# Performance work log

Measured on AMD Instinct MI355X. Metric: run time of the kernel, lower is better.

The kernel has to match this reference:

```python
import jax, jax.numpy as jnp
import numpy as np

V, TB, L, H, D, HD, FF = 50257, 1024, 6, 12, 768, 64, 4 * 768
B, T = 2, 1024
EOS = 50256


def _layernorm(x, g, b, eps=1e-5):
    mu = x.mean(-1, keepdims=True)
    var = ((x - mu) ** 2).mean(-1, keepdims=True)
    return (x - mu) * jax.lax.rsqrt(var + eps) * g + b


def setup_inputs() -> dict:
    key = jax.random.key(0)
    ks = jax.random.split(key, 10)
    resid_std = 0.02 * (2 * L) ** (-0.5)

    def n(k, shape, std=0.02):
        return (std * jax.random.normal(k, shape)).astype(jnp.float32)

    return {
        "idx": jax.random.randint(ks[0], (B, T), 0, V, dtype=jnp.int32),
        "targets": jax.random.randint(ks[1], (B, T), 0, V, dtype=jnp.int32),
        "token_emb": n(ks[2], (V, D)),           # tied with head
        "pos_emb": n(ks[3], (1, TB, D)),
        "ln1_g": jnp.ones((L, D), jnp.float32),
        "ln1_b": jnp.zeros((L, D), jnp.float32),
        "ln2_g": jnp.ones((L, D), jnp.float32),
        "ln2_b": jnp.zeros((L, D), jnp.float32),
        "W_qkv": n(ks[4], (L, D, 3 * D)),
        "b_qkv": jnp.zeros((L, 3 * D), jnp.float32),
        "W_proj": n(ks[5], (L, D, D), resid_std),
        "b_proj": jnp.zeros((L, D), jnp.float32),
        "W_fc1": n(ks[6], (L, D, FF)),
        "b_fc1": jnp.zeros((L, FF), jnp.float32),
        "W_fc2": n(ks[7], (L, FF, D), resid_std),
        "b_fc2": jnp.zeros((L, D), jnp.float32),
        "lnf_g": jnp.ones((D,), jnp.float32),
        "lnf_b": jnp.zeros((D,), jnp.float32),
    }


def reference(idx, targets, token_emb, pos_emb, ln1_g, ln1_b, ln2_g, ln2_b,
              W_qkv, b_qkv, W_proj, b_proj, W_fc1, b_fc1, W_fc2, b_fc2,
              lnf_g, lnf_b):
    Bc, Tc = idx.shape
    x = token_emb[idx] + pos_emb[:, :Tc, :]  # [B,T,D]; dropout=0 -> identity

    # document-boundary causal mask: same_doc & causal
    is_eos = (idx == EOS).astype(jnp.int32)
    doc_id = jnp.cumsum(is_eos, axis=1) - is_eos          # [B,T]
    same_doc = doc_id[:, :, None] == doc_id[:, None, :]   # [B,T,T]
    causal = jnp.tril(jnp.ones((Tc, Tc), dtype=bool))
    mask = same_doc & causal                               # [B,T,T]
    scale = 1.0 / float(np.sqrt(HD))

    def block(x, p):
        g1, b1, Wq, bq, Wp, bp, g2, b2, Wf1, bf1, Wf2, bf2 = p
        h = _layernorm(x, g1, b1)
        qkv = (h @ Wq + bq).reshape(Bc, Tc, 3, H, HD)
        q = qkv[:, :, 0].transpose(0, 2, 1, 3)  # [B,H,T,hd]
        k = qkv[:, :, 1].transpose(0, 2, 1, 3)
        v = qkv[:, :, 2].transpose(0, 2, 1, 3)
        att = jnp.einsum('bhqd,bhkd->bhqk', q, k) * scale
        att = jnp.where(mask[:, None, :, :], att, -jnp.inf)
        att = jax.nn.softmax(att, axis=-1)
        y = jnp.einsum('bhqk,bhkd->bhqd', att, v)
        y = y.transpose(0, 2, 1, 3).reshape(Bc, Tc, D)
        x = x + (y @ Wp + bp)
        h2 = _layernorm(x, g2, b2)
        x = x + (jax.nn.gelu(h2 @ Wf1 + bf1, approximate=False) @ Wf2 + bf2)
        return x, None

    x, _ = jax.lax.scan(block, x, (ln1_g, ln1_b, W_qkv, b_qkv, W_proj, b_proj,
                                   ln2_g, ln2_b, W_fc1, b_fc1, W_fc2, b_fc2))
    x = _layernorm(x, lnf_g, lnf_b)
    logits = x @ token_emb.T  # tied head, no bias
    logp = jax.nn.log_softmax(logits, axis=-1)
    tgt = targets.astype(jnp.int32)[..., None]
    loss = -jnp.take_along_axis(logp, tgt, axis=-1).mean()
    return logits, loss
```

## Files before the change

kernel.cpp:

```cpp
#include <hip/hip_runtime.h>
#include <hip/hip_bf16.h>
#include <math.h>

#define V_ 50257
#define L_ 6
#define H_ 12
#define D_ 768
#define HD_ 64
#define FF_ 3072
#define B_ 2
#define T_ 1024
#define NTOK (B_*T_)
#define EOS_ 50256
#define QBLK 64
#define KVB 64
#define NS2 393
#define QS3 (3*D_)

typedef __attribute__((ext_vector_type(8))) short s16x8;
typedef __attribute__((ext_vector_type(4))) float f32x4;

__device__ __forceinline__ short f2bf(float f) {
  __hip_bfloat16 h = __float2bfloat16(f);
  return *reinterpret_cast<short*>(&h);
}

__device__ __forceinline__ void gl_lds16(const void* g, void* l) {
  __builtin_amdgcn_global_load_lds(
      (const __attribute__((address_space(1))) unsigned int*)g,
      (__attribute__((address_space(3))) unsigned int*)l, 16, 0, 0);
}

__global__ void k_embed(const int* __restrict__ idx, const float* __restrict__ tok,
                        const float* __restrict__ pos, float* __restrict__ x) {
  int gid = blockIdx.x * blockDim.x + threadIdx.x;
  const int total = NTOK * D_;
  if (gid >= total) return;
  int row = gid / D_;
  int d = gid - row * D_;
  int t = row & (T_ - 1);
  x[gid] = tok[(size_t)idx[row] * D_ + d] + pos[t * D_ + d];
}

__global__ void k_docid(const int* __restrict__ idx, int* __restrict__ doc) {
  int b = threadIdx.x;
  if (b >= B_) return;
  int c = 0;
  for (int t = 0; t < T_; ++t) {
    int e = (idx[b*T_ + t] == EOS_) ? 1 : 0;
    doc[b*T_ + t] = c;
    c += e;
  }
}

__global__ void k_cast_tok(const float* __restrict__ in,
                           __hip_bfloat16* __restrict__ out, long n8) {
  long i = (long)blockIdx.x*blockDim.x + threadIdx.x;
  long stride = (long)gridDim.x*blockDim.x;
  for (; i < n8; i += stride) {
    const float4* src = (const float4*)(in + i*8);
    float4 v0 = src[0], v1 = src[1];
    s16x8 s;
    s[0]=f2bf(v0.x); s[1]=f2bf(v0.y); s[2]=f2bf(v0.z); s[3]=f2bf(v0.w);
    s[4]=f2bf(v1.x); s[5]=f2bf(v1.y); s[6]=f2bf(v1.z); s[7]=f2bf(v1.w);
    *(s16x8*)((short*)out + i*8) = s;
  }
}

__global__ void k_ln(const float* __restrict__ x, const float* __restrict__ g,
                     const float* __restrict__ b, __hip_bfloat16* __restrict__ out) {
  int row = blockIdx.x;
  const float* xr = x + (size_t)row * D_;
  int lane = threadIdx.x;
  float vals[D_/64];
  float s = 0.f;
  #pragma unroll
  for (int i = 0; i < D_/64; ++i) { vals[i] = xr[lane + i*64]; s += vals[i]; }
  #pragma unroll
  for (int o = 1; o < 64; o <<= 1) s += __shfl_xor(s, o);
  float mu = s * (1.f/D_);
  float v = 0.f;
  #pragma unroll
  for (int i = 0; i < D_/64; ++i) { float d0 = vals[i]-mu; v += d0*d0; }
  #pragma unroll
  for (int o = 1; o < 64; o <<= 1) v += __shfl_xor(v, o);
  float inv = rsqrtf(v * (1.f/D_) + 1e-5f);
  #pragma unroll
  for (int i = 0; i < D_/64; ++i) {
    int d = lane + i*64;
    out[(size_t)row*D_ + d] = __float2bfloat16((vals[i]-mu)*inv*g[d] + b[d]);
  }
}

__global__ void k_wt(const float* __restrict__ in, __hip_bfloat16* __restrict__ out,
                     int K, int N) {
  __shared__ float tile[32][33];
  int l = blockIdx.z;
  const float* src = in + (size_t)l*K*N;
  __hip_bfloat16* dst = out + (size_t)l*N*K;
  int n0 = blockIdx.x*32, k0 = blockIdx.y*32;
  int tx = threadIdx.x, ty = threadIdx.y;
  #pragma unroll
  for (int i = 0; i < 4; ++i)
    tile[ty + i*8][tx] = src[(size_t)(k0 + ty + i*8)*N + n0 + tx];
  __syncthreads();
  #pragma unroll
  for (int i = 0; i < 4; ++i)
    dst[(size_t)(n0 + ty + i*8)*K + k0 + tx] = __float2bfloat16(tile[tx][ty + i*8]);
}

__global__ __launch_bounds__(256) void k_mfma_nt(
    const __hip_bfloat16* __restrict__ A,
    const __hip_bfloat16* __restrict__ Bh,
    const float* __restrict__ Bf,
    const float* __restrict__ bias,
    const float* resid,
    float* outf, __hip_bfloat16* outh,
    int M, int N, int K, int gelu)
{
  __shared__ __align__(16) short lds_a[128*64];
  __shared__ __align__(16) short lds_b[128*64];
  const int t = threadIdx.x;
  const int m0 = blockIdx.y * 128;
  const int n0 = blockIdx.x * 128;
  const int lane = t & 63;
  const int wid = t >> 6;
  const int wm = (wid >> 1) * 64;
  const int wn = (wid & 1) * 64;
  const int lrow = lane & 15;
  const int lkb = (lane >> 4) * 16;
  const int wbase = (t & 192) * 16;

  f32x4 acc[4][4];
  #pragma unroll
  for (int i = 0; i < 4; ++i)
    #pragma unroll
    for (int j = 0; j < 4; ++j)
      acc[i][j] = (f32x4){0.f, 0.f, 0.f, 0.f};

  for (int k0 = 0; k0 < K; k0 += 64) {
    #pragma unroll
    for (int p = 0; p < 4; ++p) {
      int c = p*256 + t;
      int row = c >> 3;
      int colb = (c & 7) << 4;
      const char* src = (const char*)A + ((size_t)(m0+row)*K + k0)*2 + (colb ^ ((row & 7) << 4));
      gl_lds16(src, (char*)lds_a + p*4096 + wbase);
    }
    if (Bh) {
      #pragma unroll
      for (int p = 0; p < 4; ++p) {
        int c = p*256 + t;
        int row = c >> 3;
        int colb = (c & 7) << 4;
        const char* src = (const char*)Bh + ((size_t)(n0+row)*K + k0)*2 + (colb ^ ((row & 7) << 4));
        gl_lds16(src, (char*)lds_b + p*4096 + wbase);
      }
    } else {
      #pragma unroll
      for (int p = 0; p < 4; ++p) {
        int c = p*256 + t;
        int row = c >> 3;
        int colb = (c & 7) << 4;
        int gn = n0 + row;
        s16x8 s = {0,0,0,0,0,0,0,0};
        if (gn < N) {
          const char* src = (const char*)Bf + ((size_t)gn*K + k0)*4 + colb*2;
          float4 v0 = *(const float4*)src;
          float4 v1 = *(const float4*)(src + 16);
          s[0]=f2bf(v0.x); s[1]=f2bf(v0.y); s[2]=f2bf(v0.z); s[3]=f2bf(v0.w);
          s[4]=f2bf(v1.x); s[5]=f2bf(v1.y); s[6]=f2bf(v1.z); s[7]=f2bf(v1.w);
        }
        int dst = (row*128 + colb) ^ ((row & 7) << 4);
        *(s16x8*)((char*)lds_b + dst) = s;
      }
    }
    __syncthreads();
    #pragma unroll
    for (int ks = 0; ks < 2; ++ks) {
      s16x8 af[4], bfr[4];
      #pragma unroll
      for (int f = 0; f < 4; ++f) {
        int row = wm + f*16 + lrow;
        int off = (row*128 + ks*64 + lkb) ^ ((row & 7) << 4);
        af[f] = *(const s16x8*)((const char*)lds_a + off);
      }
      #pragma unroll
      for (int f = 0; f < 4; ++f) {
        int row = wn + f*16 + lrow;
        int off = (row*128 + ks*64 + lkb) ^ ((row & 7) << 4);
        bfr[f] = *(const s16x8*)((const char*)lds_b + off);
      }
      #pragma unroll
      for (int fm = 0; fm < 4; ++fm)
        #pragma unroll
        for (int fn = 0; fn < 4; ++fn)
          acc[fm][fn] = __builtin_amdgcn_mfma_f32_16x16x32_bf16(
              af[fm], bfr[fn], acc[fm][fn], 0, 0, 0);
    }
    __syncthreads();
  }
  const int crow = (lane >> 4) * 4;
  #pragma unroll
  for (int fm = 0; fm < 4; ++fm) {
    #pragma unroll
    for (int fn = 0; fn < 4; ++fn) {
      int col = n0 + wn + fn*16 + lrow;
      if (col >= N) continue;
      #pragma unroll
      for (int r = 0; r < 4; ++r) {
        int row = m0 + wm + fm*16 + crow + r;
        float v = acc[fm][fn][r];
        if (bias) v += bias[col];
        if (gelu) v = 0.5f * v * (1.f + erff(v * 0.70710678118654752f));
        if (resid) v += resid[(size_t)row*N + col];
        if (outf) outf[(size_t)row*N + col] = v;
        else      outh[(size_t)row*N + col] = __float2bfloat16(v);
      }
    }
  }
}

__global__ __launch_bounds__(256) void k_mfma_nt64(
    const __hip_bfloat16* __restrict__ A,
    const __hip_bfloat16* __restrict__ Bh,
    const float* __restrict__ bias,
    const float* resid,
    float* outf,
    int M, int N, int K)
{
  __shared__ __align__(16) short lds_a[64*64];
  __shared__ __align__(16) short lds_b[64*64];
  const int t = threadIdx.x;
  const int m0 = blockIdx.y * 64;
  const int n0 = blockIdx.x * 64;
  const int lane = t & 63;
  const int wid = t >> 6;
  const int wm = (wid >> 1) * 32;
  const int wn = (wid & 1) * 32;
  const int lrow = lane & 15;
  const int lkb = (lane >> 4) * 16;
  const int wbase = (t & 192) * 16;

  f32x4 acc[2][2];
  #pragma unroll
  for (int i = 0; i < 2; ++i)
    #pragma unroll
    for (int j = 0; j < 2; ++j)
      acc[i][j] = (f32x4){0.f, 0.f, 0.f, 0.f};

  for (int k0 = 0; k0 < K; k0 += 64) {
    #pragma unroll
    for (int p = 0; p < 2; ++p) {
      int c = p*256 + t;
      int row = c >> 3;
      int colb = (c & 7) << 4;
      const char* srcA = (const char*)A + ((size_t)(m0+row)*K + k0)*2 + (colb ^ ((row & 7) << 4));
      gl_lds16(srcA, (char*)lds_a + p*4096 + wbase);
    }
    #pragma unroll
    for (int p = 0; p < 2; ++p) {
      int c = p*256 + t;
      int row = c >> 3;
      int colb = (c & 7) << 4;
      const char* srcB = (const char*)Bh + ((size_t)(n0+row)*K + k0)*2 + (colb ^ ((row & 7) << 4));
      gl_lds16(srcB, (char*)lds_b + p*4096 + wbase);
    }
    __syncthreads();
    #pragma unroll
    for (int ks = 0; ks < 2; ++ks) {
      s16x8 af[2], bfr[2];
      #pragma unroll
      for (int f = 0; f < 2; ++f) {
        int row = wm + f*16 + lrow;
        int off = (row*128 + ks*64 + lkb) ^ ((row & 7) << 4);
        af[f] = *(const s16x8*)((const char*)lds_a + off);
      }
      #pragma unroll
      for (int f = 0; f < 2; ++f) {
        int row = wn + f*16 + lrow;
        int off = (row*128 + ks*64 + lkb) ^ ((row & 7) << 4);
        bfr[f] = *(const s16x8*)((const char*)lds_b + off);
      }
      #pragma unroll
      for (int fm = 0; fm < 2; ++fm)
        #pragma unroll
        for (int fn = 0; fn < 2; ++fn)
          acc[fm][fn] = __builtin_amdgcn_mfma_f32_16x16x32_bf16(
              af[fm], bfr[fn], acc[fm][fn], 0, 0, 0);
    }
    __syncthreads();
  }
  const int crow = (lane >> 4) * 4;
  #pragma unroll
  for (int fm = 0; fm < 2; ++fm) {
    #pragma unroll
    for (int fn = 0; fn < 2; ++fn) {
      int col = n0 + wn + fn*16 + lrow;
      #pragma unroll
      for (int r = 0; r < 4; ++r) {
        int row = m0 + wm + fm*16 + crow + r;
        float v = acc[fm][fn][r] + bias[col];
        if (resid) v += resid[(size_t)row*N + col];
        outf[(size_t)row*N + col] = v;
      }
    }
  }
}

__global__ __launch_bounds__(256) void k_logits(
    const __hip_bfloat16* __restrict__ A,
    const __hip_bfloat16* __restrict__ Bh,
    const float* __restrict__ Bf,
    float* __restrict__ C,
    float2* __restrict__ part)
{
  __shared__ __align__(16) short lds_a[128*64];
  __shared__ __align__(16) short lds_b[128*64];
  const int t = threadIdx.x;
  const int bid = blockIdx.x;
  const int lid = (bid & 7) * (NS2*16/8) + (bid >> 3);
  const int m0 = (lid & 15) * 128;
  const int nt = lid >> 4;
  const int n0 = nt * 128;
  const int lane = t & 63;
  const int wid = t >> 6;
  const int wm = (wid >> 1) * 64;
  const int wn = (wid & 1) * 64;
  const int lrow = lane & 15;
  const int lkb = (lane >> 4) * 16;
  const int wbase = (t & 192) * 16;

  f32x4 acc[4][4];
  #pragma unroll
  for (int i = 0; i < 4; ++i)
    #pragma unroll
    for (int j = 0; j < 4; ++j)
      acc[i][j] = (f32x4){0.f, 0.f, 0.f, 0.f};

  for (int k0 = 0; k0 < 768; k0 += 64) {
    #pragma unroll
    for (int p = 0; p < 4; ++p) {
      int c = p*256 + t;
      int row = c >> 3;
      int colb = (c & 7) << 4;
      const char* src = (const char*)A + ((size_t)(m0+row)*768 + k0)*2 + (colb ^ ((row & 7) << 4));
      gl_lds16(src, (char*)lds_a + p*4096 + wbase);
    }
    if (Bh) {
      #pragma unroll
      for (int p = 0; p < 4; ++p) {
        int c = p*256 + t;
        int row = c >> 3;
        int colb = (c & 7) << 4;
        const char* src = (const char*)Bh + ((size_t)(n0+row)*768 + k0)*2 + (colb ^ ((row & 7) << 4));
        gl_lds16(src, (char*)lds_b + p*4096 + wbase);
      }
    } else {
      #pragma unroll
      for (int p = 0; p < 4; ++p) {
        int c = p*256 + t;
        int row = c >> 3;
        int colb = (c & 7) << 4;
        int gn = n0 + row;
        s16x8 s = {0,0,0,0,0,0,0,0};
        if (gn < V_) {
          const char* src = (const char*)Bf + ((size_t)gn*768 + k0)*4 + colb*2;
          float4 v0 = *(const float4*)src;
          float4 v1 = *(const float4*)(src + 16);
          s[0]=f2bf(v0.x); s[1]=f2bf(v0.y); s[2]=f2bf(v0.z); s[3]=f2bf(v0.w);
          s[4]=f2bf(v1.x); s[5]=f2bf(v1.y); s[6]=f2bf(v1.z); s[7]=f2bf(v1.w);
        }
        int dst = (row*128 + colb) ^ ((row & 7) << 4);
        *(s16x8*)((char*)lds_b + dst) = s;
      }
    }
    __syncthreads();
    #pragma unroll
    for (int ks = 0; ks < 2; ++ks) {
      s16x8 af[4], bfr[4];
      #pragma unroll
      for (int f = 0; f < 4; ++f) {
        int row = wm + f*16 + lrow;
        int off = (row*128 + ks*64 + lkb) ^ ((row & 7) << 4);
        af[f] = *(const s16x8*)((const char*)lds_a + off);
      }
      #pragma unroll
      for (int f = 0; f < 4; ++f) {
        int row = wn + f*16 + lrow;
        int off = (row*128 + ks*64 + lkb) ^ ((row & 7) << 4);
        bfr[f] = *(const s16x8*)((const char*)lds_b + off);
      }
      #pragma unroll
      for (int fm = 0; fm < 4; ++fm)
        #pragma unroll
        for (int fn = 0; fn < 4; ++fn)
          acc[fm][fn] = __builtin_amdgcn_mfma_f32_16x16x32_bf16(
              af[fm], bfr[fn], acc[fm][fn], 0, 0, 0);
    }
    __syncthreads();
  }
  const int crow = (lane >> 4) * 4;
  bool valid[4];
  #pragma unroll
  for (int fn = 0; fn < 4; ++fn) valid[fn] = (n0 + wn + fn*16 + lrow) < V_;
  float2* red = (float2*)lds_a;
  #pragma unroll
  for (int fm = 0; fm < 4; ++fm) {
    #pragma unroll
    for (int r = 0; r < 4; ++r) {
      int rit = wm + fm*16 + crow + r;
      int row = m0 + rit;
      float m = -1e30f;
      #pragma unroll
      for (int fn = 0; fn < 4; ++fn) {
        if (valid[fn]) {
          float v = acc[fm][fn][r];
          __builtin_nontemporal_store(v, &C[(size_t)row*V_ + n0 + wn + fn*16 + lrow]);
          m = fmaxf(m, v);
        }
      }
      #pragma unroll
      for (int o = 1; o < 16; o <<= 1) m = fmaxf(m, __shfl_xor(m, o));
      float s = 0.f;
      #pragma unroll
      for (int fn = 0; fn < 4; ++fn)
        if (valid[fn]) s += __expf(acc[fm][fn][r] - m);
      #pragma unroll
      for (int o = 1; o < 16; o <<= 1) s += __shfl_xor(s, o);
      if (lrow == 0) red[rit*2 + (wid & 1)] = make_float2(m, s);
    }
  }
  __syncthreads();
  if (t < 128) {
    float2 a = red[t*2], b = red[t*2 + 1];
    float mn = fmaxf(a.x, b.x);
    float S = a.y*__expf(a.x - mn) + b.y*__expf(b.x - mn);
    part[(size_t)(m0 + t)*NS2 + nt] = make_float2(mn, S);
  }
}

__global__ void k_rowloss2(const float2* __restrict__ part,
                           const float* __restrict__ logits,
                           const int* __restrict__ tgt, float* __restrict__ rl) {
  int row = blockIdx.x;
  int lane = threadIdx.x;
  float M = -1e30f, S = 0.f;
  for (int i = lane; i < NS2; i += 64) {
    float2 p = part[(size_t)row*NS2 + i];
    float mn = fmaxf(M, p.x);
    S = S*__expf(M - mn) + p.y*__expf(p.x - mn);
    M = mn;
  }
  #pragma unroll
  for (int o = 1; o < 64; o <<= 1) {
    float Mo = __shfl_xor(M, o);
    float So = __shfl_xor(S, o);
    float mn = fmaxf(M, Mo);
    S = S*__expf(M - mn) + So*__expf(Mo - mn);
    M = mn;
  }
  if (lane == 0)
    rl[row] = (logf(S) + M) - logits[(size_t)row*V_ + tgt[row]];
}

__global__ __launch_bounds__(256) void k_fattn(
    const __hip_bfloat16* __restrict__ qkv, const int* __restrict__ doc,
    __hip_bfloat16* __restrict__ y)
{
  __shared__ __align__(16) short q_lds[QBLK*64];
  __shared__ __align__(16) short k_lds[KVB*64];
  __shared__ __align__(16) short vt_lds[64*KVB];
  __shared__ __align__(16) short p_lds[4][16*64];
  __shared__ int doc_k[KVB];
  const int t = threadIdx.x;
  const int lane = t & 63;
  const int w = t >> 6;
  const int q0 = blockIdx.x * QBLK;
  const int h = blockIdx.y, b = blockIdx.z;
  const int lrow = lane & 15;
  const int lgrp = lane >> 4;
  const int crow = lgrp * 4;
  const int wbase = (t & 192) * 16;
  const short* qp = (const short*)qkv;

  #pragma unroll
  for (int p = 0; p < 2; ++p) {
    int c = p*256 + t;
    int row = c >> 3;
    int colb = (c & 7) << 4;
    const char* src = (const char*)(qp + ((size_t)(b*T_ + q0 + row))*QS3 + h*HD_)
                      + (colb ^ ((row & 7) << 4));
    gl_lds16(src, (char*)q_lds + p*4096 + wbase);
  }
  int docq[4];
  #pragma unroll
  for (int r = 0; r < 4; ++r)
    docq[r] = doc[b*T_ + q0 + w*16 + crow + r];
  __syncthreads();

  float m_r[4], l_r[4];
  #pragma unroll
  for (int r = 0; r < 4; ++r) { m_r[r] = -1e30f; l_r[r] = 0.f; }
  f32x4 o[4];
  #pragma unroll
  for (int fd = 0; fd < 4; ++fd) o[fd] = (f32x4){0.f,0.f,0.f,0.f};

  const int ntiles = q0/KVB + 1;
  for (int kt = 0; kt < ntiles; ++kt) {
    const int kv0 = kt * KVB;
    #pragma unroll
    for (int p = 0; p < 2; ++p) {
      int c = p*256 + t;
      int row = c >> 3;
      int colb = (c & 7) << 4;
      const char* src = (const char*)(qp + ((size_t)(b*T_ + kv0 + row))*QS3 + D_ + h*HD_)
                        + (colb ^ ((row & 7) << 4));
      gl_lds16(src, (char*)k_lds + p*4096 + wbase);
    }
    #pragma unroll
    for (int p = 0; p < 2; ++p) {
      int c = p*256 + t;
      int kvr = c >> 3, d0 = (c & 7)*8;
      s16x8 s = *(const s16x8*)(qp + ((size_t)(b*T_ + kv0 + kvr))*QS3 + 2*D_ + h*HD_ + d0);
      #pragma unroll
      for (int j = 0; j < 8; ++j) {
        int d = d0 + j;
        int off = (d*128 + kvr*2) ^ ((d & 7) << 4);
        *(short*)((char*)vt_lds + off) = s[j];
      }
    }
    if (t < KVB) doc_k[t] = doc[b*T_ + kv0 + t];
    __syncthreads();

    f32x4 sfr[4];
    #pragma unroll
    for (int fn = 0; fn < 4; ++fn) sfr[fn] = (f32x4){0.f,0.f,0.f,0.f};
    #pragma unroll
    for (int ks = 0; ks < 2; ++ks) {
      int arow = w*16 + lrow;
      s16x8 af = *(const s16x8*)((const char*)q_lds +
                 ((arow*128 + lgrp*16 + ks*64) ^ ((arow & 7) << 4)));
      #pragma unroll
      for (int fn = 0; fn < 4; ++fn) {
        int brow = fn*16 + lrow;
        s16x8 bf = *(const s16x8*)((const char*)k_lds +
                   ((brow*128 + lgrp*16 + ks*64) ^ ((brow & 7) << 4)));
        sfr[fn] = __builtin_amdgcn_mfma_f32_16x16x32_bf16(af, bf, sfr[fn], 0, 0, 0);
      }
    }
    int dk[4];
    #pragma unroll
    for (int fn = 0; fn < 4; ++fn) dk[fn] = doc_k[fn*16 + lrow];
    float rowmax[4] = {-1e30f, -1e30f, -1e30f, -1e30f};
    #pragma unroll
    for (int fn = 0; fn < 4; ++fn) {
      int col = kv0 + fn*16 + lrow;
      #pragma unroll
      for (int r = 0; r < 4; ++r) {
        int qrow = q0 + w*16 + crow + r;
        bool ok = (col <= qrow) && (dk[fn] == docq[r]);
        float v = ok ? sfr[fn][r] * 0.125f : -1e30f;
        sfr[fn][r] = v;
        rowmax[r] = fmaxf(rowmax[r], v);
      }
    }
    #pragma unroll
    for (int r = 0; r < 4; ++r) {
      float v = rowmax[r];
      #pragma unroll
      for (int off = 1; off < 16; off <<= 1) v = fmaxf(v, __shfl_xor(v, off));
      rowmax[r] = v;
    }
    float alpha[4], psum[4];
    #pragma unroll
    for (int r = 0; r < 4; ++r) {
      float mn = fmaxf(m_r[r], rowmax[r]);
      alpha[r] = __expf(m_r[r] - mn);
      m_r[r] = mn;
      psum[r] = 0.f;
    }
    #pragma unroll
    for (int fn = 0; fn < 4; ++fn) {
      #pragma unroll
      for (int r = 0; r < 4; ++r) {
        float sv = sfr[fn][r];
        float p = (sv < -5e29f) ? 0.f : __expf(sv - m_r[r]);
        psum[r] += p;
        int rl_ = crow + r;
        int off = (rl_*128 + (fn*16 + lrow)*2) ^ ((rl_ & 7) << 4);
        *(short*)((char*)p_lds[w] + off) = f2bf(p);
      }
    }
    #pragma unroll
    for (int r = 0; r < 4; ++r) {
      float v = psum[r];
      #pragma unroll
      for (int off = 1; off < 16; off <<= 1) v += __shfl_xor(v, off);
      l_r[r] = l_r[r]*alpha[r] + v;
    }
    #pragma unroll
    for (int fd = 0; fd < 4; ++fd)
      #pragma unroll
      for (int r = 0; r < 4; ++r)
        o[fd][r] *= alpha[r];
    __syncthreads();
    #pragma unroll
    for (int ks = 0; ks < 2; ++ks) {
      s16x8 af = *(const s16x8*)((const char*)p_lds[w] +
                 ((lrow*128 + lgrp*16 + ks*64) ^ ((lrow & 7) << 4)));
      #pragma unroll
      for (int fd = 0; fd < 4; ++fd) {
        int brow = fd*16 + lrow;
        s16x8 bf = *(const s16x8*)((const char*)vt_lds +
                   ((brow*128 + lgrp*16 + ks*64) ^ ((brow & 7) << 4)));
        o[fd] = __builtin_amdgcn_mfma_f32_16x16x32_bf16(af, bf, o[fd], 0, 0, 0);
      }
    }
    __syncthreads();
  }
  #pragma unroll
  for (int r = 0; r < 4; ++r) {
    float inv = 1.f / l_r[r];
    int rowg = b*T_ + q0 + w*16 + crow + r;
    #pragma unroll
    for (int fd = 0; fd < 4; ++fd) {
      int col = h*HD_ + fd*16 + lrow;
      y[(size_t)rowg*D_ + col] = __float2bfloat16(o[fd][r] * inv);
    }
  }
}

__global__ void k_rowloss(const float* __restrict__ logits,
                          const int* __restrict__ tgt, float* __restrict__ rl) {
  __shared__ float red[4];
  int row = blockIdx.x;
  const float* lr = logits + (size_t)row * V_;
  int tid = threadIdx.x;
  float m = -1e30f;
  for (int v = tid; v < V_; v += 256) m = fmaxf(m, lr[v]);
  #pragma unroll
  for (int o = 1; o < 64; o <<= 1) m = fmaxf(m, __shfl_xor(m, o));
  if ((tid & 63) == 0) red[tid >> 6] = m;
  __syncthreads();
  m = fmaxf(fmaxf(red[0], red[1]), fmaxf(red[2], red[3]));
  __syncthreads();
  float s = 0.f;
  for (int v = tid; v < V_; v += 256) s += __expf(lr[v] - m);
  #pragma unroll
  for (int o = 1; o < 64; o <<= 1) s += __shfl_xor(s, o);
  if ((tid & 63) == 0) red[tid >> 6] = s;
  __syncthreads();
  if (tid == 0) {
    s = red[0]+red[1]+red[2]+red[3];
    rl[row] = (logf(s) + m) - lr[tgt[row]];
  }
}

__global__ void k_loss(const float* __restrict__ rl, float* __restrict__ out) {
  __shared__ float red[4];
  int tid = threadIdx.x;
  float s = 0.f;
  for (int i = tid; i < NTOK; i += 256) s += rl[i];
  #pragma unroll
  for (int o = 1; o < 64; o <<= 1) s += __shfl_xor(s, o);
  if ((tid & 63) == 0) red[tid >> 6] = s;
  __syncthreads();
  if (tid == 0) {
    s = red[0]+red[1]+red[2]+red[3];
    out[0] = s / (float)NTOK;
  }
}

extern "C" void kernel_launch(void* const* d_in, const int* in_sizes, int n_in,
                              void* d_out, int out_size, void* d_ws, size_t ws_size,
                              hipStream_t stream) {
  const int*   idx   = (const int*)d_in[0];
  const int*   tgt   = (const int*)d_in[1];
  const float* tok   = (const float*)d_in[2];
  const float* pos   = (const float*)d_in[3];
  const float* ln1_g = (const float*)d_in[4];
  const float* ln1_b = (const float*)d_in[5];
  const float* ln2_g = (const float*)d_in[6];
  const float* ln2_b = (const float*)d_in[7];
  const float* W_qkv = (const float*)d_in[8];
  const float* b_qkv = (const float*)d_in[9];
  const float* W_proj= (const float*)d_in[10];
  const float* b_proj= (const float*)d_in[11];
  const float* W_fc1 = (const float*)d_in[12];
  const float* b_fc1 = (const float*)d_in[13];
  const float* W_fc2 = (const float*)d_in[14];
  const float* b_fc2 = (const float*)d_in[15];
  const float* lnf_g = (const float*)d_in[16];
  const float* lnf_b = (const float*)d_in[17];

  float* out = (float*)d_out;

  char* ob = (char*)d_out;
  float*           x    = (float*)(ob + 0);
  __hip_bfloat16*  qkv  = (__hip_bfloat16*)(ob + (size_t)6291456);
  __hip_bfloat16*  y    = (__hip_bfloat16*)(ob + (size_t)15728640);
  __hip_bfloat16*  tff  = (__hip_bfloat16*)(ob + (size_t)18874368);
  __hip_bfloat16*  WTq  = (__hip_bfloat16*)(ob + (size_t)40894464);
  __hip_bfloat16*  WTp  = (__hip_bfloat16*)(ob + (size_t)62128128);
  __hip_bfloat16*  WT1  = (__hip_bfloat16*)(ob + (size_t)69206016);
  __hip_bfloat16*  WT2  = (__hip_bfloat16*)(ob + (size_t)97517568);

  char* wb = (char*)d_ws;
  __hip_bfloat16* h    = (__hip_bfloat16*)(wb + 0);
  int*    doc  = (int*)  (wb + (size_t)3145728);
  float*  rl   = (float*)(wb + (size_t)3153920);
  float2* part = (float2*)(wb + (size_t)3162112);
  __hip_bfloat16* tokh = (__hip_bfloat16*)(wb + (size_t)9601024);
  const size_t ws_need_part = (size_t)9601024;
  const size_t ws_need_tokh = (size_t)9601024 + 77194752 + 131072;
  const bool fused_loss = (ws_size >= ws_need_part);
  const bool use_tokh   = (ws_size >= ws_need_tokh);

  dim3 tb(32, 8);
  k_wt<<<dim3(2304/32, 768/32, L_), tb, 0, stream>>>(W_qkv,  WTq,  768, 2304);
  k_wt<<<dim3( 768/32, 768/32, L_), tb, 0, stream>>>(W_proj, WTp,  768,  768);
  k_wt<<<dim3(3072/32, 768/32, L_), tb, 0, stream>>>(W_fc1,  WT1,  768, 3072);
  k_wt<<<dim3( 768/32,3072/32, L_), tb, 0, stream>>>(W_fc2,  WT2, 3072,  768);
  if (use_tokh)
    k_cast_tok<<<2048, 256, 0, stream>>>(tok, tokh, (long)V_*768/8);

  k_embed<<<(NTOK*D_ + 255)/256, 256, 0, stream>>>(idx, tok, pos, x);
  k_docid<<<1, 64, 0, stream>>>(idx, doc);

  for (int l = 0; l < L_; ++l) {
    k_ln<<<NTOK, 64, 0, stream>>>(x, ln1_g + l*D_, ln1_b + l*D_, h);
    k_mfma_nt<<<dim3(2304/128, NTOK/128), 256, 0, stream>>>(
        h, WTq + (size_t)l*2304*768, nullptr, b_qkv + (size_t)l*2304, nullptr,
        nullptr, qkv, NTOK, 2304, 768, 0);
    k_fattn<<<dim3(T_/QBLK, H_, B_), 256, 0, stream>>>(qkv, doc, y);
    k_mfma_nt64<<<dim3(768/64, NTOK/64), 256, 0, stream>>>(
        y, WTp + (size_t)l*768*768, b_proj + (size_t)l*768, x, x,
        NTOK, 768, 768);
    k_ln<<<NTOK, 64, 0, stream>>>(x, ln2_g + l*D_, ln2_b + l*D_, h);
    k_mfma_nt<<<dim3(3072/128, NTOK/128), 256, 0, stream>>>(
        h, WT1 + (size_t)l*3072*768, nullptr, b_fc1 + (size_t)l*3072, nullptr,
        nullptr, tff, NTOK, 3072, 768, 1);
    k_mfma_nt64<<<dim3(768/64, NTOK/64), 256, 0, stream>>>(
        tff, WT2 + (size_t)l*768*3072, b_fc2 + (size_t)l*768, x, x,
        NTOK, 768, 3072);
  }
  k_ln<<<NTOK, 64, 0, stream>>>(x, lnf_g, lnf_b, h);

  if (fused_loss) {
    k_logits<<<NS2*16, 256, 0, stream>>>(
        h, use_tokh ? tokh : nullptr, tok, out, part);
    k_rowloss2<<<NTOK, 64, 0, stream>>>(part, out, tgt, rl);
  } else {
    k_mfma_nt<<<dim3((V_ + 127)/128, NTOK/128), 256, 0, stream>>>(
        h, nullptr, tok, nullptr, nullptr, out, nullptr, NTOK, V_, 768, 0);
    k_rowloss<<<NTOK, 256, 0, stream>>>(out, tgt, rl);
  }
  k_loss<<<1, 256, 0, stream>>>(rl, out + (size_t)NTOK*V_);
}
```

Baseline: 1.599 ms.

## Double-buffer GEMM LDS tiles, vectorize layernorm, reverse attention block order

All three MFMA GEMM kernels (k_mfma_nt, k_mfma_nt64, k_logits) now double-buffer their LDS tiles. They prefetch the tile two steps ahead with async global-to-LDS loads and use explicit vmcnt waits instead of a full sync on every k-step. Layernorm now processes four rows per 256-thread block with float4 loads and packed bf16 stores. Flash attention launches the heaviest causal query blocks first and drops one barrier before the PV MFMA. The price is double the LDS per block, which may lower occupancy. The hand-counted vmcnt thresholds and the removed barrier are fragile points for races.

```diff
diff --git a/kernel.cpp b/kernel.cpp
--- a/kernel.cpp
+++ b/kernel.cpp
@@ -18,6 +18,7 @@
 #define QS3 (3*D_)
 
 typedef __attribute__((ext_vector_type(8))) short s16x8;
+typedef __attribute__((ext_vector_type(4))) short s16x4;
 typedef __attribute__((ext_vector_type(4))) float f32x4;
 
 __device__ __forceinline__ short f2bf(float f) {
@@ -67,28 +68,42 @@
   }
 }
 
-__global__ void k_ln(const float* __restrict__ x, const float* __restrict__ g,
-                     const float* __restrict__ b, __hip_bfloat16* __restrict__ out) {
-  int row = blockIdx.x;
+__global__ __launch_bounds__(256) void k_ln(
+    const float* __restrict__ x, const float* __restrict__ g,
+    const float* __restrict__ b, __hip_bfloat16* __restrict__ out) {
+  int row = blockIdx.x * 4 + (threadIdx.x >> 6);
+  int lane = threadIdx.x & 63;
   const float* xr = x + (size_t)row * D_;
-  int lane = threadIdx.x;
-  float vals[D_/64];
+  float4 v[3];
   float s = 0.f;
   #pragma unroll
-  for (int i = 0; i < D_/64; ++i) { vals[i] = xr[lane + i*64]; s += vals[i]; }
+  for (int i = 0; i < 3; ++i) {
+    v[i] = *(const float4*)(xr + lane*4 + i*256);
+    s += v[i].x + v[i].y + v[i].z + v[i].w;
+  }
   #pragma unroll
   for (int o = 1; o < 64; o <<= 1) s += __shfl_xor(s, o);
   float mu = s * (1.f/D_);
-  float v = 0.f;
-  #pragma unroll
-  for (int i = 0; i < D_/64; ++i) { float d0 = vals[i]-mu; v += d0*d0; }
-  #pragma unroll
-  for (int o = 1; o < 64; o <<= 1) v += __shfl_xor(v, o);
-  float inv = rsqrtf(v * (1.f/D_) + 1e-5f);
-  #pragma unroll
-  for (int i = 0; i < D_/64; ++i) {
-    int d = lane + i*64;
-    out[(size_t)row*D_ + d] = __float2bfloat16((vals[i]-mu)*inv*g[d] + b[d]);
+  float var = 0.f;
+  #pragma unroll
+  for (int i = 0; i < 3; ++i) {
+    float a0=v[i].x-mu, a1=v[i].y-mu, a2=v[i].z-mu, a3=v[i].w-mu;
+    var += a0*a0 + a1*a1 + a2*a2 + a3*a3;
+  }
+  #pragma unroll
+  for (int o = 1; o < 64; o <<= 1) var += __shfl_xor(var, o);
+  float inv = rsqrtf(var * (1.f/D_) + 1e-5f);
+  #pragma unroll
+  for (int i = 0; i < 3; ++i) {
+    int d = lane*4 + i*256;
+    float4 gg = *(const float4*)(g + d);
+    float4 bb = *(const float4*)(b + d);
+    s16x4 o4;
+    o4[0] = f2bf((v[i].x-mu)*inv*gg.x + bb.x);
+    o4[1] = f2bf((v[i].y-mu)*inv*gg.y + bb.y);
+    o4[2] = f2bf((v[i].z-mu)*inv*gg.z + bb.z);
+    o4[3] = f2bf((v[i].w-mu)*inv*gg.w + bb.w);
+    *(s16x4*)((short*)out + (size_t)row*D_ + d) = o4;
   }
 }
 
@@ -118,8 +133,8 @@
     float* outf, __hip_bfloat16* outh,
     int M, int N, int K, int gelu)
 {
-  __shared__ __align__(16) short lds_a[128*64];
-  __shared__ __align__(16) short lds_b[128*64];
+  __shared__ __align__(16) short lds_a[2][128*64];
+  __shared__ __align__(16) short lds_b[2][128*64];
   const int t = threadIdx.x;
   const int m0 = blockIdx.y * 128;
   const int n0 = blockIdx.x * 128;
@@ -131,22 +146,17 @@
   const int lkb = (lane >> 4) * 16;
   const int wbase = (t & 192) * 16;
 
-  f32x4 acc[4][4];
-  #pragma unroll
-  for (int i = 0; i < 4; ++i)
-    #pragma unroll
-    for (int j = 0; j < 4; ++j)
-      acc[i][j] = (f32x4){0.f, 0.f, 0.f, 0.f};
-
-  for (int k0 = 0; k0 < K; k0 += 64) {
+  auto stageA = [&](int buf, int k0) {
     #pragma unroll
     for (int p = 0; p < 4; ++p) {
       int c = p*256 + t;
       int row = c >> 3;
       int colb = (c & 7) << 4;
       const char* src = (const char*)A + ((size_t)(m0+row)*K + k0)*2 + (colb ^ ((row & 7) << 4));
-      gl_lds16(src, (char*)lds_a + p*4096 + wbase);
-    }
+      gl_lds16(src, (char*)lds_a[buf] + p*4096 + wbase);
+    }
+  };
+  auto stageB = [&](int buf, int k0) {
     if (Bh) {
       #pragma unroll
       for (int p = 0; p < 4; ++p) {
@@ -154,7 +164,7 @@
         int row = c >> 3;
         int colb = (c & 7) << 4;
         const char* src = (const char*)Bh + ((size_t)(n0+row)*K + k0)*2 + (colb ^ ((row & 7) << 4));
-        gl_lds16(src, (char*)lds_b + p*4096 + wbase);
+        gl_lds16(src, (char*)lds_b[buf] + p*4096 + wbase);
       }
     } else {
       #pragma unroll
@@ -172,10 +182,27 @@
           s[4]=f2bf(v1.x); s[5]=f2bf(v1.y); s[6]=f2bf(v1.z); s[7]=f2bf(v1.w);
         }
         int dst = (row*128 + colb) ^ ((row & 7) << 4);
-        *(s16x8*)((char*)lds_b + dst) = s;
-      }
-    }
-    __syncthreads();
+        *(s16x8*)((char*)lds_b[buf] + dst) = s;
+      }
+    }
+  };
+
+  f32x4 acc[4][4];
+  #pragma unroll
+  for (int i = 0; i < 4; ++i)
+    #pragma unroll
+    for (int j = 0; j < 4; ++j)
+      acc[i][j] = (f32x4){0.f, 0.f, 0.f, 0.f};
+
+  const int nk = K >> 6;
+  stageA(0, 0); stageB(0, 0);
+  stageA(1, 64); stageB(1, 64);
+  const bool piped = (Bh != nullptr);
+  for (int kt = 0; kt < nk; ++kt) {
+    if (piped && kt + 1 < nk) asm volatile("s_waitcnt vmcnt(8)" ::: "memory");
+    else                      asm volatile("s_waitcnt vmcnt(0) lgkmcnt(0)" ::: "memory");
+    __builtin_amdgcn_s_barrier();
+    const int cur = kt & 1;
     #pragma unroll
     for (int ks = 0; ks < 2; ++ks) {
       s16x8 af[4], bfr[4];
@@ -183,13 +210,13 @@
       for (int f = 0; f < 4; ++f) {
         int row = wm + f*16 + lrow;
         int off = (row*128 + ks*64 + lkb) ^ ((row & 7) << 4);
-        af[f] = *(const s16x8*)((const char*)lds_a + off);
+        af[f] = *(const s16x8*)((const char*)lds_a[cur] + off);
       }
       #pragma unroll
       for (int f = 0; f < 4; ++f) {
         int row = wn + f*16 + lrow;
         int off = (row*128 + ks*64 + lkb) ^ ((row & 7) << 4);
-        bfr[f] = *(const s16x8*)((const char*)lds_b + off);
+        bfr[f] = *(const s16x8*)((const char*)lds_b[cur] + off);
       }
       #pragma unroll
       for (int fm = 0; fm < 4; ++fm)
@@ -198,7 +225,8 @@
           acc[fm][fn] = __builtin_amdgcn_mfma_f32_16x16x32_bf16(
               af[fm], bfr[fn], acc[fm][fn], 0, 0, 0);
     }
-    __syncthreads();
+    __builtin_amdgcn_s_barrier();
+    if (kt + 2 < nk) { stageA(cur, (kt+2)*64); stageB(cur, (kt+2)*64); }
   }
   const int crow = (lane >> 4) * 4;
   #pragma unroll
@@ -229,8 +257,8 @@
     float* outf,
     int M, int N, int K)
 {
-  __shared__ __align__(16) short lds_a[64*64];
-  __shared__ __align__(16) short lds_b[64*64];
+  __shared__ __align__(16) short lds_a[2][64*64];
+  __shared__ __align__(16) short lds_b[2][64*64];
   const int t = threadIdx.x;
   const int m0 = blockIdx.y * 64;
   const int n0 = blockIdx.x * 64;
@@ -242,21 +270,14 @@
   const int lkb = (lane >> 4) * 16;
   const int wbase = (t & 192) * 16;
 
-  f32x4 acc[2][2];
-  #pragma unroll
-  for (int i = 0; i < 2; ++i)
-    #pragma unroll
-    for (int j = 0; j < 2; ++j)
-      acc[i][j] = (f32x4){0.f, 0.f, 0.f, 0.f};
-
-  for (int k0 = 0; k0 < K; k0 += 64) {
+  auto stage = [&](int buf, int k0) {
     #pragma unroll
     for (int p = 0; p < 2; ++p) {
       int c = p*256 + t;
       int row = c >> 3;
       int colb = (c & 7) << 4;
       const char* srcA = (const char*)A + ((size_t)(m0+row)*K + k0)*2 + (colb ^ ((row & 7) << 4));
-      gl_lds16(srcA, (char*)lds_a + p*4096 + wbase);
+      gl_lds16(srcA, (char*)lds_a[buf] + p*4096 + wbase);
     }
     #pragma unroll
     for (int p = 0; p < 2; ++p) {
@@ -264,9 +285,25 @@
       int row = c >> 3;
       int colb = (c & 7) << 4;
       const char* srcB = (const char*)Bh + ((size_t)(n0+row)*K + k0)*2 + (colb ^ ((row & 7) << 4));
-      gl_lds16(srcB, (char*)lds_b + p*4096 + wbase);
-    }
-    __syncthreads();
+      gl_lds16(srcB, (char*)lds_b[buf] + p*4096 + wbase);
+    }
+  };
+
+  f32x4 acc[2][2];
+  #pragma unroll
+  for (int i = 0; i < 2; ++i)
+    #pragma unroll
+    for (int j = 0; j < 2; ++j)
+      acc[i][j] = (f32x4){0.f, 0.f, 0.f, 0.f};
+
+  const int nk = K >> 6;
+  stage(0, 0);
+  stage(1, 64);
+  for (int kt = 0; kt < nk; ++kt) {
+    if (kt + 1 < nk) asm volatile("s_waitcnt vmcnt(4)" ::: "memory");
+    else             asm volatile("s_waitcnt vmcnt(0)" ::: "memory");
+    __builtin_amdgcn_s_barrier();
+    const int cur = kt & 1;
     #pragma unroll
     for (int ks = 0; ks < 2; ++ks) {
       s16x8 af[2], bfr[2];
@@ -274,13 +311,13 @@
       for (int f = 0; f < 2; ++f) {
         int row = wm + f*16 + lrow;
         int off = (row*128 + ks*64 + lkb) ^ ((row & 7) << 4);
-        af[f] = *(const s16x8*)((const char*)lds_a + off);
+        af[f] = *(const s16x8*)((const char*)lds_a[cur] + off);
       }
       #pragma unroll
       for (int f = 0; f < 2; ++f) {
         int row = wn + f*16 + lrow;
         int off = (row*128 + ks*64 + lkb) ^ ((row & 7) << 4);
-        bfr[f] = *(const s16x8*)((const char*)lds_b + off);
+        bfr[f] = *(const s16x8*)((const char*)lds_b[cur] + off);
       }
       #pragma unroll
       for (int fm = 0; fm < 2; ++fm)
@@ -289,7 +326,8 @@
           acc[fm][fn] = __builtin_amdgcn_mfma_f32_16x16x32_bf16(
               af[fm], bfr[fn], acc[fm][fn], 0, 0, 0);
     }
-    __syncthreads();
+    __builtin_amdgcn_s_barrier();
+    if (kt + 2 < nk) stage(cur, (kt+2)*64);
   }
   const int crow = (lane >> 4) * 4;
   #pragma unroll
@@ -315,8 +353,8 @@
     float* __restrict__ C,
     float2* __restrict__ part)
 {
-  __shared__ __align__(16) short lds_a[128*64];
-  __shared__ __align__(16) short lds_b[128*64];
+  __shared__ __align__(16) short lds_a[2][128*64];
+  __shared__ __align__(16) short lds_b[2][128*64];
   const int t = threadIdx.x;
   const int bid = blockIdx.x;
   const int lid = (bid & 7) * (NS2*16/8) + (bid >> 3);
@@ -331,22 +369,17 @@
   const int lkb = (lane >> 4) * 16;
   const int wbase = (t & 192) * 16;
 
-  f32x4 acc[4][4];
-  #pragma unroll
-  for (int i = 0; i < 4; ++i)
-    #pragma unroll
-    for (int j = 0; j < 4; ++j)
-      acc[i][j] = (f32x4){0.f, 0.f, 0.f, 0.f};
-
-  for (int k0 = 0; k0 < 768; k0 += 64) {
+  auto stageA = [&](int buf, int k0) {
     #pragma unroll
     for (int p = 0; p < 4; ++p) {
       int c = p*256 + t;
       int row = c >> 3;
       int colb = (c & 7) << 4;
       const char* src = (const char*)A + ((size_t)(m0+row)*768 + k0)*2 + (colb ^ ((row & 7) << 4));
-      gl_lds16(src, (char*)lds_a + p*4096 + wbase);
-    }
+      gl_lds16(src, (char*)lds_a[buf] + p*4096 + wbase);
+    }
+  };
+  auto stageB = [&](int buf, int k0) {
     if (Bh) {
       #pragma unroll
       for (int p = 0; p < 4; ++p) {
@@ -354,7 +387,7 @@
         int row = c >> 3;
         int colb = (c & 7) << 4;
         const char* src = (const char*)Bh + ((size_t)(n0+row)*768 + k0)*2 + (colb ^ ((row & 7) << 4));
-        gl_lds16(src, (char*)lds_b + p*4096 + wbase);
+        gl_lds16(src, (char*)lds_b[buf] + p*4096 + wbase);
       }
     } else {
       #pragma unroll
@@ -372,10 +405,26 @@
           s[4]=f2bf(v1.x); s[5]=f2bf(v1.y); s[6]=f2bf(v1.z); s[7]=f2bf(v1.w);
         }
         int dst = (row*128 + colb) ^ ((row & 7) << 4);
-        *(s16x8*)((char*)lds_b + dst) = s;
-      }
-    }
-    __syncthreads();
+        *(s16x8*)((char*)lds_b[buf] + dst) = s;
+      }
+    }
+  };
+
+  f32x4 acc[4][4];
+  #pragma unroll
+  for (int i = 0; i < 4; ++i)
+    #pragma unroll
+    for (int j = 0; j < 4; ++j)
+      acc[i][j] = (f32x4){0.f, 0.f, 0.f, 0.f};
+
+  stageA(0, 0); stageB(0, 0);
+  stageA(1, 64); stageB(1, 64);
+  const bool piped = (Bh != nullptr);
+  for (int kt = 0; kt < 12; ++kt) {
+    if (piped && kt + 1 < 12) asm volatile("s_waitcnt vmcnt(8)" ::: "memory");
+    else                      asm volatile("s_waitcnt vmcnt(0) lgkmcnt(0)" ::: "memory");
+    __builtin_amdgcn_s_barrier();
+    const int cur = kt & 1;
     #pragma unroll
     for (int ks = 0; ks < 2; ++ks) {
       s16x8 af[4], bfr[4];
@@ -383,13 +432,13 @@
       for (int f = 0; f < 4; ++f) {
         int row = wm + f*16 + lrow;
         int off = (row*128 + ks*64 + lkb) ^ ((row & 7) << 4);
-        af[f] = *(const s16x8*)((const char*)lds_a + off);
+        af[f] = *(const s16x8*)((const char*)lds_a[cur] + off);
       }
       #pragma unroll
       for (int f = 0; f < 4; ++f) {
         int row = wn + f*16 + lrow;
         int off = (row*128 + ks*64 + lkb) ^ ((row & 7) << 4);
-        bfr[f] = *(const s16x8*)((const char*)lds_b + off);
+        bfr[f] = *(const s16x8*)((const char*)lds_b[cur] + off);
       }
       #pragma unroll
       for (int fm = 0; fm < 4; ++fm)
@@ -398,7 +447,8 @@
           acc[fm][fn] = __builtin_amdgcn_mfma_f32_16x16x32_bf16(
               af[fm], bfr[fn], acc[fm][fn], 0, 0, 0);
     }
-    __syncthreads();
+    __builtin_amdgcn_s_barrier();
+    if (kt + 2 < 12) { stageA(cur, (kt+2)*64); stageB(cur, (kt+2)*64); }
   }
   const int crow = (lane >> 4) * 4;
   bool valid[4];
@@ -476,7 +526,7 @@
   const int t = threadIdx.x;
   const int lane = t & 63;
   const int w = t >> 6;
-  const int q0 = blockIdx.x * QBLK;
+  const int q0 = (gridDim.x - 1 - blockIdx.x) * QBLK;
   const int h = blockIdx.y, b = blockIdx.z;
   const int lrow = lane & 15;
   const int lgrp = lane >> 4;
@@ -604,7 +654,6 @@
       #pragma unroll
       for (int r = 0; r < 4; ++r)
         o[fd][r] *= alpha[r];
-    __syncthreads();
     #pragma unroll
     for (int ks = 0; ks < 2; ++ks) {
       s16x8 af = *(const s16x8*)((const char*)p_lds[w] +
@@ -729,7 +778,7 @@
   k_docid<<<1, 64, 0, stream>>>(idx, doc);
 
   for (int l = 0; l < L_; ++l) {
-    k_ln<<<NTOK, 64, 0, stream>>>(x, ln1_g + l*D_, ln1_b + l*D_, h);
+    k_ln<<<NTOK/4, 256, 0, stream>>>(x, ln1_g + l*D_, ln1_b + l*D_, h);
     k_mfma_nt<<<dim3(2304/128, NTOK/128), 256, 0, stream>>>(
         h, WTq + (size_t)l*2304*768, nullptr, b_qkv + (size_t)l*2304, nullptr,
         nullptr, qkv, NTOK, 2304, 768, 0);
@@ -737,7 +786,7 @@
     k_mfma_nt64<<<dim3(768/64, NTOK/64), 256, 0, stream>>>(
         y, WTp + (size_t)l*768*768, b_proj + (size_t)l*768, x, x,
         NTOK, 768, 768);
-    k_ln<<<NTOK, 64, 0, stream>>>(x, ln2_g + l*D_, ln2_b + l*D_, h);
+    k_ln<<<NTOK/4, 256, 0, stream>>>(x, ln2_g + l*D_, ln2_b + l*D_, h);
     k_mfma_nt<<<dim3(3072/128, NTOK/128), 256, 0, stream>>>(
         h, WT1 + (size_t)l*3072*768, nullptr, b_fc1 + (size_t)l*3072, nullptr,
         nullptr, tff, NTOK, 3072, 768, 1);
@@ -745,7 +794,7 @@
         tff, WT2 + (size_t)l*768*3072, b_fc2 + (size_t)l*768, x, x,
         NTOK, 768, 3072);
   }
-  k_ln<<<NTOK, 64, 0, stream>>>(x, lnf_g, lnf_b, h);
+  k_ln<<<NTOK/4, 256, 0, stream>>>(x, lnf_g, lnf_b, h);
 
   if (fused_loss) {
     k_logits<<<NS2*16, 256, 0, stream>>>(
```

Result: no change. 1.570 ms (-1.8%).
